# Performance work log

Measured on AMD Instinct MI355X. Metric: run time of the kernel, lower is better.

## Reference

```python
import jax, jax.numpy as jnp
import numpy as np


def _gcn(x, src, dst, W, b, M):
    # GCNConv: out = D^{-1/2} (A+I) D^{-1/2} X W + b, messages flow src->dst
    xw = x @ W  # [M, D]
    loops = jnp.arange(M)
    s = jnp.concatenate([src, loops])
    d = jnp.concatenate([dst, loops])
    deg = jax.ops.segment_sum(jnp.ones_like(s, x.dtype), d, num_segments=M)
    dinv = jnp.where(deg > 0, jax.lax.rsqrt(jnp.maximum(deg, 1.0)), 0.0)
    norm = dinv[s] * dinv[d]  # [Eg+M]
    return jax.ops.segment_sum(norm[:, None] * xw[s], d, num_segments=M) + b


def _graph_cross_attention(values, k, q, e_src, e_dst, N):
    # gather-dot, segment softmax over destination tokens, scatter-sum of values
    scale = jnp.sqrt(jnp.asarray(k.shape[1], k.dtype))
    dots = (q[e_dst] * k[e_src]).sum(-1) / scale  # [Ea]
    m = jax.ops.segment_max(dots, e_dst, num_segments=N)
    m = jnp.where(jnp.isfinite(m), m, 0.0)
    w = jnp.exp(dots - m[e_dst])
    den = jax.ops.segment_sum(w, e_dst, num_segments=N)
    w = w / jnp.where(den > 0, den, 1.0)[e_dst]
    return jax.ops.segment_sum(w[:, None] * values[e_src], e_dst, num_segments=N)


def reference(token_embeddings, tokens2edges, edge_index, e2t_src, e2t_dst,
              W_gnn, b_gnn, Wk, bk, Wq, bq, Wl, bl, gate_a, gate_b):
    N = token_embeddings.shape[1]
    M = tokens2edges.shape[1]

    def per_sample(t, t2e, ei, es, ed):
        edge_emb = t[t2e]                                  # [M, D] gather
        edge_emb = _gcn(edge_emb, ei[0], ei[1], W_gnn, b_gnn, M)
        k = edge_emb @ Wk + bk                             # [M, 64]
        q = t @ Wq + bq                                    # [N, 64]
        gatt = _graph_cross_attention(edge_emb, k, q, es, ed, N)  # [N, D]
        new = t + jnp.tanh(gate_a) * gatt
        new = new + jnp.tanh(gate_b) * (new @ Wl + bl)
        return new

    return jax.vmap(per_sample)(token_embeddings, tokens2edges, edge_index, e2t_src, e2t_dst)


def setup_inputs() -> dict:
    B, N, M, Eg, Ea, D, DK = 4, 4096, 16384, 65536, 65536, 512, 64
    key = jax.random.key(0)
    ks = jax.random.split(key, 16)
    s = 0.05  # weight scale to keep activations well-conditioned
    return {
        "token_embeddings": jax.random.normal(ks[0], (B, N, D), jnp.float32),
        "tokens2edges": jax.random.randint(ks[1], (B, M), 0, N),
        "edge_index": jax.random.randint(ks[2], (B, 2, Eg), 0, M),
        "e2t_src": jax.random.randint(ks[3], (B, Ea), 0, M),
        "e2t_dst": jax.random.randint(ks[4], (B, Ea), 0, N),
        "W_gnn": jax.random.normal(ks[5], (D, D), jnp.float32) * s,
        "b_gnn": jax.random.normal(ks[6], (D,), jnp.float32) * s,
        "Wk": jax.random.normal(ks[7], (D, DK), jnp.float32) * s,
        "bk": jax.random.normal(ks[8], (DK,), jnp.float32) * s,
        "Wq": jax.random.normal(ks[9], (D, DK), jnp.float32) * s,
        "bq": jax.random.normal(ks[10], (DK,), jnp.float32) * s,
        "Wl": jax.random.normal(ks[11], (D, D), jnp.float32) * s,
        "bl": jax.random.normal(ks[12], (D,), jnp.float32) * s,
        "gate_a": jax.random.normal(ks[13], (1,), jnp.float32),
        "gate_b": jax.random.normal(ks[14], (1,), jnp.float32),
    }
```

## Files before the change

### kernel.cpp

```cpp
#include <hip/hip_runtime.h>
#include <math.h>

#define BB 4
#define NT 4096
#define ME 16384
#define EG 65536
#define EA 65536
#define DD 512
#define DKK 64

using bf16x8 = __attribute__((ext_vector_type(8))) short;
using f32x4  = __attribute__((ext_vector_type(4))) float;

static __device__ __forceinline__ unsigned short f2bf(float f) {
    unsigned u = __float_as_uint(f);
    u += 0x7fffu + ((u >> 16) & 1u);
    return (unsigned short)(u >> 16);
}
static __device__ __forceinline__ float bf2f(unsigned short u) {
    return __uint_as_float((unsigned)u << 16);
}
static __device__ __forceinline__ void acc8(float* a, uint4 v, float s) {
    a[0] += s * __uint_as_float(v.x << 16);
    a[1] += s * __uint_as_float(v.x & 0xffff0000u);
    a[2] += s * __uint_as_float(v.y << 16);
    a[3] += s * __uint_as_float(v.y & 0xffff0000u);
    a[4] += s * __uint_as_float(v.z << 16);
    a[5] += s * __uint_as_float(v.z & 0xffff0000u);
    a[6] += s * __uint_as_float(v.w << 16);
    a[7] += s * __uint_as_float(v.w & 0xffff0000u);
}
static __device__ __forceinline__ uint4 pack8(const float* a) {
    uint4 o;
    o.x = (unsigned)f2bf(a[0]) | ((unsigned)f2bf(a[1]) << 16);
    o.y = (unsigned)f2bf(a[2]) | ((unsigned)f2bf(a[3]) << 16);
    o.z = (unsigned)f2bf(a[4]) | ((unsigned)f2bf(a[5]) << 16);
    o.w = (unsigned)f2bf(a[6]) | ((unsigned)f2bf(a[7]) << 16);
    return o;
}

__global__ void k_hist2(const int* __restrict__ ei_all, const int* __restrict__ ed_all,
                        int* __restrict__ cntG, int* __restrict__ cntA) {
    int i = blockIdx.x * 256 + threadIdx.x;
    if (i < BB * EG) {
        int b = i >> 16, e = i & (EG - 1);
        int dst = ei_all[(size_t)b * 2 * EG + EG + e];
        atomicAdd(&cntG[b * ME + dst], 1);
    } else {
        int j = i - BB * EG;
        atomicAdd(&cntA[(j >> 16) * NT + ed_all[j]], 1);
    }
}

__global__ __launch_bounds__(1024) void k_scan2(
    const int* __restrict__ cntG, int* __restrict__ offsG, int* __restrict__ curG,
    float* __restrict__ dinv,
    const int* __restrict__ cntA, int* __restrict__ offsA, int* __restrict__ curA) {
    __shared__ int sums[1024];
    int tid = threadIdx.x;
    int bid = blockIdx.x;
    const int* cnt;
    int *offs, *cur;
    float* dv = nullptr;
    int C, nk;
    if (bid < BB) {
        cnt = cntG + bid * ME; offs = offsG + bid * (ME + 1); cur = curG + bid * ME;
        dv = dinv + bid * ME; C = ME / 1024; nk = ME;
    } else {
        int b = bid - BB;
        cnt = cntA + b * NT; offs = offsA + b * (NT + 1); cur = curA + b * NT;
        C = NT / 1024; nk = NT;
    }
    int local[16];
    int tot = 0;
    for (int i = 0; i < C; ++i) { local[i] = cnt[tid * C + i]; tot += local[i]; }
    sums[tid] = tot;
    __syncthreads();
    for (int d = 1; d < 1024; d <<= 1) {
        int v = (tid >= d) ? sums[tid - d] : 0;
        __syncthreads();
        sums[tid] += v;
        __syncthreads();
    }
    int run = sums[tid] - tot;
    for (int i = 0; i < C; ++i) {
        int idx = tid * C + i;
        offs[idx] = run;
        cur[idx] = run;
        if (dv) dv[idx] = rsqrtf((float)local[i] + 1.0f);
        run += local[i];
    }
    if (tid == 1023) offs[nk] = run;
}

__global__ void k_fill2(const int* __restrict__ ei_all, const int* __restrict__ es_all,
                        const int* __restrict__ ed_all, const int* __restrict__ t2e_all,
                        const float* __restrict__ dinv,
                        int* __restrict__ curG, int2* __restrict__ csrG,
                        int* __restrict__ curA, int2* __restrict__ csrA) {
    int i = blockIdx.x * 256 + threadIdx.x;
    if (i < BB * EG) {
        int b = i >> 16, e = i & (EG - 1);
        const int* ei = ei_all + (size_t)b * 2 * EG;
        int s = ei[e], d = ei[EG + e];
        int p = atomicAdd(&curG[b * ME + d], 1);
        int2 v;
        v.x = t2e_all[(b << 14) + s];
        v.y = __float_as_int(dinv[b * ME + s]);
        csrG[(size_t)b * EG + p] = v;
    } else {
        int j = i - BB * EG;
        int b = j >> 16;
        int p = atomicAdd(&curA[b * NT + ed_all[j]], 1);
        int2 v;
        v.x = es_all[j];
        v.y = ed_all[j];
        csrA[(size_t)b * EA + p] = v;
    }
}

__global__ void k_cast(const float* __restrict__ x, unsigned short* __restrict__ xb) {
    long i = (long)blockIdx.x * blockDim.x + threadIdx.x;
    float4 v = *(const float4*)(x + (i << 2));
    ushort4 o;
    o.x = f2bf(v.x); o.y = f2bf(v.y); o.z = f2bf(v.z); o.w = f2bf(v.w);
    *(ushort4*)(xb + (i << 2)) = o;
}

__global__ void k_wt(const float* __restrict__ W, unsigned short* __restrict__ Wt) {
    int i = blockIdx.x * 256 + threadIdx.x;
    int n = i >> 9, k = i & 511;
    Wt[i] = f2bf(W[((long)k << 9) + n]);
}
__global__ void k_wtT(const float* __restrict__ Wgnn, const float* __restrict__ Wgk,
                      const float* __restrict__ Wq, unsigned short* __restrict__ BtT) {
    int i = blockIdx.x * 256 + threadIdx.x;
    int n = i >> 9, k = i & 511;
    float v;
    if (n < 512)      v = Wgnn[((long)k << 9) + n];
    else if (n < 576) v = Wgk[k * 64 + (n - 512)];
    else              v = Wq[k * 64 + (n - 576)];
    BtT[i] = f2bf(v);
}
__global__ void k_bias(const float* __restrict__ bgnn, const float* __restrict__ Wk,
                       const float* __restrict__ bk, const float* __restrict__ bq,
                       float* __restrict__ biasG, float* __restrict__ bias640) {
    int tid = threadIdx.x;
    if (tid < 512) { biasG[tid] = bgnn[tid]; bias640[tid] = 0.0f; return; }
    if (tid < 576) {
        int n = tid - 512;
        float s = bk[n];
        for (int k = 0; k < DD; ++k) s += bgnn[k] * Wk[k * 64 + n];
        biasG[tid] = s;
        bias640[tid] = 0.0f;
        return;
    }
    bias640[tid] = bq[tid - 576];
}

__global__ __launch_bounds__(256, 2) void gemm_token(
    const unsigned short* __restrict__ A, const unsigned short* __restrict__ BtT,
    const float* __restrict__ bias640, unsigned short* __restrict__ Xg,
    unsigned short* __restrict__ Xk, unsigned short* __restrict__ qmatb)
{
    __shared__ short As[64 * 32];
    __shared__ short Bs[320 * 32];
    int tid = threadIdx.x;
    int lane = tid & 63;
    int w = tid >> 6;
    long bm = (long)blockIdx.x * 64;
    int bcol = blockIdx.y * 320;
    const unsigned short* Bblk = BtT + (long)bcol * DD;

    f32x4 acc[4][5] = {};

    for (int k0 = 0; k0 < DD; k0 += 32) {
        {
            int s = tid;
            int r = s >> 2;
            int gc = ((s & 3) ^ ((s >> 3) & 3)) * 8;
            __builtin_amdgcn_global_load_lds(
                (const __attribute__((address_space(1))) unsigned int*)(A + (bm + r) * DD + k0 + gc),
                (__attribute__((address_space(3))) unsigned int*)(As + s * 8), 16, 0, 0);
        }
#pragma unroll
        for (int i = 0; i < 5; ++i) {
            int s = tid + i * 256;
            int r = s >> 2;
            int gc = ((s & 3) ^ ((s >> 3) & 3)) * 8;
            __builtin_amdgcn_global_load_lds(
                (const __attribute__((address_space(1))) unsigned int*)(Bblk + (long)r * DD + k0 + gc),
                (__attribute__((address_space(3))) unsigned int*)(Bs + s * 8), 16, 0, 0);
        }
        __syncthreads();

        int cq = lane >> 4;
        bf16x8 af[4];
#pragma unroll
        for (int rb = 0; rb < 4; ++rb) {
            int r = rb * 16 + (lane & 15);
            af[rb] = *(const bf16x8*)&As[(r * 4 + (cq ^ ((r >> 1) & 3))) * 8];
        }
#pragma unroll
        for (int cb = 0; cb < 5; ++cb) {
            int r = w * 80 + cb * 16 + (lane & 15);
            bf16x8 bf = *(const bf16x8*)&Bs[(r * 4 + (cq ^ ((r >> 1) & 3))) * 8];
#pragma unroll
            for (int rb = 0; rb < 4; ++rb)
                acc[rb][cb] = __builtin_amdgcn_mfma_f32_16x16x32_bf16(af[rb], bf, acc[rb][cb], 0, 0, 0);
        }
        __syncthreads();
    }

#pragma unroll
    for (int rb = 0; rb < 4; ++rb) {
        long row0 = bm + rb * 16 + ((lane >> 4) << 2);
#pragma unroll
        for (int cb = 0; cb < 5; ++cb) {
            int col = bcol + w * 80 + cb * 16 + (lane & 15);
            float bv = bias640[col];
            if (col < 512) {
#pragma unroll
                for (int r = 0; r < 4; ++r)
                    Xg[(row0 + r) * DD + col] = f2bf(acc[rb][cb][r] + bv);
            } else if (col < 576) {
#pragma unroll
                for (int r = 0; r < 4; ++r)
                    Xk[(row0 + r) * DKK + (col - 512)] = f2bf(acc[rb][cb][r] + bv);
            } else {
#pragma unroll
                for (int r = 0; r < 4; ++r)
                    qmatb[(row0 + r) * DKK + (col - 576)] = f2bf(acc[rb][cb][r] + bv);
            }
        }
    }
}

__global__ __launch_bounds__(256) void k_gcn_gather(
    const unsigned short* __restrict__ Xg, const unsigned short* __restrict__ Xk,
    const int* __restrict__ t2e_all, const float* __restrict__ dinv,
    const int* __restrict__ offsG, const int2* __restrict__ csrG,
    const float* __restrict__ biasG,
    unsigned short* __restrict__ eeb, unsigned short* __restrict__ kmatb)
{
    int mg = (blockIdx.x * 256 + threadIdx.x) >> 6;
    int lane = threadIdx.x & 63;
    int b = mg >> 14;
    int m = mg & (ME - 1);
    const int* offs = offsG + b * (ME + 1);
    const int2* csr = csrG + (size_t)b * EG;
    const unsigned short* gl = Xg + (((long)b * NT) << 9) + lane * 8;
    const unsigned short* kl = Xk + ((long)b * NT) * DKK + lane;

    float dm = dinv[mg];
    int self = t2e_all[mg];
    uint4 vself = *(const uint4*)(gl + ((long)self << 9));
    float kself = bf2f(kl[(long)self * DKK]);

    float a[8] = {0, 0, 0, 0, 0, 0, 0, 0};
    float ak = 0.0f;
    int p = offs[m], end = offs[m + 1];
    for (; p + 4 <= end; p += 4) {
        int2 e0 = csr[p], e1 = csr[p + 1], e2 = csr[p + 2], e3 = csr[p + 3];
        uint4 r0 = *(const uint4*)(gl + ((long)e0.x << 9));
        uint4 r1 = *(const uint4*)(gl + ((long)e1.x << 9));
        uint4 r2 = *(const uint4*)(gl + ((long)e2.x << 9));
        uint4 r3 = *(const uint4*)(gl + ((long)e3.x << 9));
        float k0 = bf2f(kl[(long)e0.x * DKK]);
        float k1 = bf2f(kl[(long)e1.x * DKK]);
        float k2 = bf2f(kl[(long)e2.x * DKK]);
        float k3 = bf2f(kl[(long)e3.x * DKK]);
        float w0 = __int_as_float(e0.y), w1 = __int_as_float(e1.y);
        float w2 = __int_as_float(e2.y), w3 = __int_as_float(e3.y);
        acc8(a, r0, w0); ak += w0 * k0;
        acc8(a, r1, w1); ak += w1 * k1;
        acc8(a, r2, w2); ak += w2 * k2;
        acc8(a, r3, w3); ak += w3 * k3;
    }
    if (p < end) {
        int e1m = end - 1;
        int i1 = min(p + 1, e1m), i2 = min(p + 2, e1m), i3 = min(p + 3, e1m);
        int2 e0 = csr[p], e1 = csr[i1], e2 = csr[i2], e3 = csr[i3];
        uint4 r0 = *(const uint4*)(gl + ((long)e0.x << 9));
        uint4 r1 = *(const uint4*)(gl + ((long)e1.x << 9));
        uint4 r2 = *(const uint4*)(gl + ((long)e2.x << 9));
        uint4 r3 = *(const uint4*)(gl + ((long)e3.x << 9));
        float k0 = bf2f(kl[(long)e0.x * DKK]);
        float k1 = bf2f(kl[(long)e1.x * DKK]);
        float k2 = bf2f(kl[(long)e2.x * DKK]);
        float k3 = bf2f(kl[(long)e3.x * DKK]);
        float w0 = __int_as_float(e0.y);
        float w1 = (p + 1 < end) ? __int_as_float(e1.y) : 0.0f;
        float w2 = (p + 2 < end) ? __int_as_float(e2.y) : 0.0f;
        float w3 = (p + 3 < end) ? __int_as_float(e3.y) : 0.0f;
        acc8(a, r0, w0); ak += w0 * k0;
        acc8(a, r1, w1); ak += w1 * k1;
        acc8(a, r2, w2); ak += w2 * k2;
        acc8(a, r3, w3); ak += w3 * k3;
    }
    acc8(a, vself, dm);
    ak += dm * kself;

    const float* bg = biasG + lane * 8;
    float4 b0 = *(const float4*)bg;
    float4 b1 = *(const float4*)(bg + 4);
    a[0] = dm * a[0] + b0.x; a[1] = dm * a[1] + b0.y;
    a[2] = dm * a[2] + b0.z; a[3] = dm * a[3] + b0.w;
    a[4] = dm * a[4] + b1.x; a[5] = dm * a[5] + b1.y;
    a[6] = dm * a[6] + b1.z; a[7] = dm * a[7] + b1.w;
    *(uint4*)(eeb + ((long)mg << 9) + lane * 8) = pack8(a);
    kmatb[(long)mg * DKK + lane] = f2bf(dm * ak + biasG[512 + lane]);
}

__global__ void k_dots(const unsigned short* __restrict__ kmatb,
                       const unsigned short* __restrict__ qmatb,
                       const int2* __restrict__ csrA, int2* __restrict__ swbuf) {
    int p = blockIdx.x * 256 + threadIdx.x;
    int b = p >> 16;
    int2 sd = csrA[p];
    const uint4* kr = (const uint4*)(kmatb + ((long)(b * ME + sd.x) << 6));
    const uint4* qr = (const uint4*)(qmatb + ((long)(b * NT + sd.y) << 6));
    float dot = 0.0f;
#pragma unroll
    for (int j = 0; j < 8; ++j) {
        uint4 kv = kr[j];
        uint4 qv = qr[j];
        dot += __uint_as_float(kv.x << 16) * __uint_as_float(qv.x << 16)
             + __uint_as_float(kv.x & 0xffff0000u) * __uint_as_float(qv.x & 0xffff0000u)
             + __uint_as_float(kv.y << 16) * __uint_as_float(qv.y << 16)
             + __uint_as_float(kv.y & 0xffff0000u) * __uint_as_float(qv.y & 0xffff0000u)
             + __uint_as_float(kv.z << 16) * __uint_as_float(qv.z << 16)
             + __uint_as_float(kv.z & 0xffff0000u) * __uint_as_float(qv.z & 0xffff0000u)
             + __uint_as_float(kv.w << 16) * __uint_as_float(qv.w << 16)
             + __uint_as_float(kv.w & 0xffff0000u) * __uint_as_float(qv.w & 0xffff0000u);
    }
    int2 o;
    o.x = sd.x;
    o.y = __float_as_int(expf(dot * 0.125f));
    swbuf[p] = o;
}

__global__ __launch_bounds__(256) void k_att_gather(
    const unsigned short* __restrict__ eeb, const int2* __restrict__ swbuf,
    const int* __restrict__ offsA,
    const float* __restrict__ t_all, const float* __restrict__ ga,
    float* __restrict__ out, unsigned short* __restrict__ nb)
{
    int ng = (blockIdx.x * 256 + threadIdx.x) >> 6;
    int lane = threadIdx.x & 63;
    int b = ng >> 12;
    int n = ng & (NT - 1);
    const int* offs = offsA + b * (NT + 1);
    const int2* swb = swbuf + (size_t)b * EA;
    const unsigned short* el = eeb + (((size_t)b * ME) << 9) + lane * 8;

    float a[8] = {0, 0, 0, 0, 0, 0, 0, 0};
    float den = 0.0f;
    int p = offs[n], end = offs[n + 1];
    for (; p + 8 <= end; p += 8) {
        int2 e0 = swb[p],     e1 = swb[p + 1], e2 = swb[p + 2], e3 = swb[p + 3];
        int2 e4 = swb[p + 4], e5 = swb[p + 5], e6 = swb[p + 6], e7 = swb[p + 7];
        uint4 r0 = *(const uint4*)(el + ((long)e0.x << 9));
        uint4 r1 = *(const uint4*)(el + ((long)e1.x << 9));
        uint4 r2 = *(const uint4*)(el + ((long)e2.x << 9));
        uint4 r3 = *(const uint4*)(el + ((long)e3.x << 9));
        uint4 r4 = *(const uint4*)(el + ((long)e4.x << 9));
        uint4 r5 = *(const uint4*)(el + ((long)e5.x << 9));
        uint4 r6 = *(const uint4*)(el + ((long)e6.x << 9));
        uint4 r7 = *(const uint4*)(el + ((long)e7.x << 9));
        float w0 = __int_as_float(e0.y), w1 = __int_as_float(e1.y);
        float w2 = __int_as_float(e2.y), w3 = __int_as_float(e3.y);
        float w4 = __int_as_float(e4.y), w5 = __int_as_float(e5.y);
        float w6 = __int_as_float(e6.y), w7 = __int_as_float(e7.y);
        den += (w0 + w1 + w2 + w3) + (w4 + w5 + w6 + w7);
        acc8(a, r0, w0);
        acc8(a, r1, w1);
        acc8(a, r2, w2);
        acc8(a, r3, w3);
        acc8(a, r4, w4);
        acc8(a, r5, w5);
        acc8(a, r6, w6);
        acc8(a, r7, w7);
    }
    if (p < end) {
        int e1m = end - 1;
        int2 e0 = swb[p];
        int2 e1 = swb[min(p + 1, e1m)];
        int2 e2 = swb[min(p + 2, e1m)];
        int2 e3 = swb[min(p + 3, e1m)];
        int2 e4 = swb[min(p + 4, e1m)];
        int2 e5 = swb[min(p + 5, e1m)];
        int2 e6 = swb[min(p + 6, e1m)];
        int2 e7 = swb[min(p + 7, e1m)];
        uint4 r0 = *(const uint4*)(el + ((long)e0.x << 9));
        uint4 r1 = *(const uint4*)(el + ((long)e1.x << 9));
        uint4 r2 = *(const uint4*)(el + ((long)e2.x << 9));
        uint4 r3 = *(const uint4*)(el + ((long)e3.x << 9));
        uint4 r4 = *(const uint4*)(el + ((long)e4.x << 9));
        uint4 r5 = *(const uint4*)(el + ((long)e5.x << 9));
        uint4 r6 = *(const uint4*)(el + ((long)e6.x << 9));
        uint4 r7 = *(const uint4*)(el + ((long)e7.x << 9));
        float w0 = __int_as_float(e0.y);
        float w1 = (p + 1 < end) ? __int_as_float(e1.y) : 0.0f;
        float w2 = (p + 2 < end) ? __int_as_float(e2.y) : 0.0f;
        float w3 = (p + 3 < end) ? __int_as_float(e3.y) : 0.0f;
        float w4 = (p + 4 < end) ? __int_as_float(e4.y) : 0.0f;
        float w5 = (p + 5 < end) ? __int_as_float(e5.y) : 0.0f;
        float w6 = (p + 6 < end) ? __int_as_float(e6.y) : 0.0f;
        float w7 = (p + 7 < end) ? __int_as_float(e7.y) : 0.0f;
        den += (w0 + w1 + w2 + w3) + (w4 + w5 + w6 + w7);
        acc8(a, r0, w0);
        acc8(a, r1, w1);
        acc8(a, r2, w2);
        acc8(a, r3, w3);
        acc8(a, r4, w4);
        acc8(a, r5, w5);
        acc8(a, r6, w6);
        acc8(a, r7, w7);
    }
    float g = tanhf(ga[0]);
    float inv = den > 0.0f ? g / den : 0.0f;
    const float* tr = t_all + ((long)ng << 9) + lane * 8;
    float4 t0 = *(const float4*)tr;
    float4 t1 = *(const float4*)(tr + 4);
    float o[8];
    o[0] = t0.x + inv * a[0]; o[1] = t0.y + inv * a[1];
    o[2] = t0.z + inv * a[2]; o[3] = t0.w + inv * a[3];
    o[4] = t1.x + inv * a[4]; o[5] = t1.y + inv * a[5];
    o[6] = t1.z + inv * a[6]; o[7] = t1.w + inv * a[7];
    float* op = out + ((long)ng << 9) + lane * 8;
    *(float4*)op = make_float4(o[0], o[1], o[2], o[3]);
    *(float4*)(op + 4) = make_float4(o[4], o[5], o[6], o[7]);
    *(uint4*)(nb + ((long)ng << 9) + lane * 8) = pack8(o);
}

__global__ __launch_bounds__(256, 2) void gemm_final(
    const unsigned short* __restrict__ A, const unsigned short* __restrict__ Bt,
    const float* __restrict__ bias, float* __restrict__ Cf, const float* __restrict__ gs)
{
    constexpr int CB = 8;
    constexpr int BROWS = 2 * CB * 16;
    __shared__ short As[128 * 32];
    __shared__ short Bs[BROWS * 32];
    int tid = threadIdx.x;
    int lane = tid & 63;
    int w = tid >> 6;
    int wm = w >> 1, wn = w & 1;
    long bm = (long)blockIdx.x * 128;
    int bcol = blockIdx.y * BROWS;
    const unsigned short* Bblk = Bt + (long)bcol * DD;

    f32x4 acc[4][CB] = {};

    for (int k0 = 0; k0 < DD; k0 += 32) {
#pragma unroll
        for (int i = 0; i < 2; ++i) {
            int s = tid + i * 256;
            int r = s >> 2;
            int gc = ((s & 3) ^ ((s >> 3) & 3)) * 8;
            __builtin_amdgcn_global_load_lds(
                (const __attribute__((address_space(1))) unsigned int*)(A + (bm + r) * DD + k0 + gc),
                (__attribute__((address_space(3))) unsigned int*)(As + s * 8), 16, 0, 0);
        }
#pragma unroll
        for (int i = 0; i < CB / 2; ++i) {
            int s = tid + i * 256;
            int r = s >> 2;
            int gc = ((s & 3) ^ ((s >> 3) & 3)) * 8;
            __builtin_amdgcn_global_load_lds(
                (const __attribute__((address_space(1))) unsigned int*)(Bblk + (long)r * DD + k0 + gc),
                (__attribute__((address_space(3))) unsigned int*)(Bs + s * 8), 16, 0, 0);
        }
        __syncthreads();

        int cq = lane >> 4;
        bf16x8 af[4];
#pragma unroll
        for (int rb = 0; rb < 4; ++rb) {
            int r = wm * 64 + rb * 16 + (lane & 15);
            af[rb] = *(const bf16x8*)&As[(r * 4 + (cq ^ ((r >> 1) & 3))) * 8];
        }
#pragma unroll
        for (int cb = 0; cb < CB; ++cb) {
            int r = wn * (CB * 16) + cb * 16 + (lane & 15);
            bf16x8 bf = *(const bf16x8*)&Bs[(r * 4 + (cq ^ ((r >> 1) & 3))) * 8];
#pragma unroll
            for (int rb = 0; rb < 4; ++rb)
                acc[rb][cb] = __builtin_amdgcn_mfma_f32_16x16x32_bf16(af[rb], bf, acc[rb][cb], 0, 0, 0);
        }
        __syncthreads();
    }

    float g = tanhf(gs[0]);
#pragma unroll
    for (int rb = 0; rb < 4; ++rb) {
        long row0 = bm + wm * 64 + rb * 16 + ((lane >> 4) << 2);
#pragma unroll
        for (int cb = 0; cb < CB; ++cb) {
            int col = bcol + wn * (CB * 16) + cb * 16 + (lane & 15);
            float bv = bias[col];
#pragma unroll
            for (int r = 0; r < 4; ++r)
                Cf[(row0 + r) * DD + col] += g * (acc[rb][cb][r] + bv);
        }
    }
}

__global__ void gemm_tiled(const float* __restrict__ A, const float* __restrict__ Bw,
                           float* __restrict__ C, int K, int Nc) {
    __shared__ float As[16][64];
    __shared__ float Bs[16][64];
    int tid = threadIdx.x;
    int tx = tid & 15, ty = tid >> 4;
    int bm = blockIdx.x * 64, bn = blockIdx.y * 64;
    float acc[4][4] = {};
    int arow = bm + (tid >> 2);
    long aoff = (long)arow * K;
    int kk0 = (tid & 3) * 4;
    int arowl = tid >> 2;
    for (int k0 = 0; k0 < K; k0 += 16) {
        float4 av = *(const float4*)(A + aoff + k0 + kk0);
        As[kk0 + 0][arowl] = av.x;
        As[kk0 + 1][arowl] = av.y;
        As[kk0 + 2][arowl] = av.z;
        As[kk0 + 3][arowl] = av.w;
        float4 bv = *(const float4*)(Bw + (long)(k0 + (tid >> 4)) * Nc + bn + (tid & 15) * 4);
        *(float4*)&Bs[tid >> 4][(tid & 15) * 4] = bv;
        __syncthreads();
#pragma unroll
        for (int k = 0; k < 16; ++k) {
            float4 a = *(const float4*)&As[k][ty * 4];
            float4 b = *(const float4*)&Bs[k][tx * 4];
            acc[0][0] += a.x * b.x; acc[0][1] += a.x * b.y; acc[0][2] += a.x * b.z; acc[0][3] += a.x * b.w;
            acc[1][0] += a.y * b.x; acc[1][1] += a.y * b.y; acc[1][2] += a.y * b.z; acc[1][3] += a.y * b.w;
            acc[2][0] += a.z * b.x; acc[2][1] += a.z * b.y; acc[2][2] += a.z * b.z; acc[2][3] += a.z * b.w;
            acc[3][0] += a.w * b.x; acc[3][1] += a.w * b.y; acc[3][2] += a.w * b.z; acc[3][3] += a.w * b.w;
        }
        __syncthreads();
    }
#pragma unroll
    for (int i = 0; i < 4; ++i)
        *(float4*)(C + (long)(bm + ty * 4 + i) * Nc + bn + tx * 4) =
            make_float4(acc[i][0], acc[i][1], acc[i][2], acc[i][3]);
}

extern "C" void kernel_launch(void* const* d_in, const int* in_sizes, int n_in,
                              void* d_out, int out_size, void* d_ws, size_t ws_size,
                              hipStream_t stream) {
    const float* t_all   = (const float*)d_in[0];
    const int*   t2e_all = (const int*)d_in[1];
    const int*   ei_all  = (const int*)d_in[2];
    const int*   es_all  = (const int*)d_in[3];
    const int*   ed_all  = (const int*)d_in[4];
    const float* Wgnn    = (const float*)d_in[5];
    const float* bgnn    = (const float*)d_in[6];
    const float* Wk      = (const float*)d_in[7];
    const float* bk      = (const float*)d_in[8];
    const float* Wq      = (const float*)d_in[9];
    const float* bq      = (const float*)d_in[10];
    const float* Wl      = (const float*)d_in[11];
    const float* bl      = (const float*)d_in[12];
    const float* ga      = (const float*)d_in[13];
    const float* gb      = (const float*)d_in[14];
    float* out = (float*)d_out;

    char* wsb = (char*)d_ws;
    size_t off = 0;
    unsigned short* eeb   = (unsigned short*)(wsb + off); off += (size_t)BB * ME * DD * 2;
    unsigned short* tb    = (unsigned short*)(wsb + off); off += (size_t)BB * NT * DD * 2;
    unsigned short* Xg    = (unsigned short*)(wsb + off); off += (size_t)BB * NT * DD * 2;
    unsigned short* nb    = (unsigned short*)(wsb + off); off += (size_t)BB * NT * DD * 2;
    unsigned short* Xk    = (unsigned short*)(wsb + off); off += (size_t)BB * NT * DKK * 2;
    unsigned short* qmatb = (unsigned short*)(wsb + off); off += (size_t)BB * NT * DKK * 2;
    unsigned short* kmatb = (unsigned short*)(wsb + off); off += (size_t)BB * ME * DKK * 2;
    unsigned short* BtT   = (unsigned short*)(wsb + off); off += (size_t)640 * DD * 2;
    unsigned short* Wlt   = (unsigned short*)(wsb + off); off += (size_t)DD * DD * 2;
    float* Wgk     = (float*)(wsb + off); off += (size_t)DD * DKK * 4;
    float* biasG   = (float*)(wsb + off); off += 576 * 4;
    float* bias640 = (float*)(wsb + off); off += 640 * 4;
    float* dinv  = (float*)(wsb + off); off += (size_t)BB * ME * 4;
    int2* swbuf  = (int2*)(wsb + off); off += (size_t)BB * EA * 8;
    int* cntG  = (int*)(wsb + off); off += (size_t)BB * ME * 4;
    int* cntA  = (int*)(wsb + off); off += (size_t)BB * NT * 4;
    int* offsG = (int*)(wsb + off); off += (size_t)BB * (ME + 1) * 4;
    int* curG  = (int*)(wsb + off); off += (size_t)BB * ME * 4;
    int2* csrG = (int2*)(wsb + off); off += (size_t)BB * EG * 8;
    int* offsA = (int*)(wsb + off); off += (size_t)BB * (NT + 1) * 4;
    int* curA  = (int*)(wsb + off); off += (size_t)BB * NT * 4;
    int2* csrA = (int2*)(wsb + off); off += (size_t)BB * EA * 8;

    gemm_tiled<<<dim3(DD / 64, 1), 256, 0, stream>>>(Wgnn, Wk, Wgk, DD, DKK);
    k_wt<<<(DD * DD) / 256, 256, 0, stream>>>(Wl, Wlt);
    k_wtT<<<(640 * DD) / 256, 256, 0, stream>>>(Wgnn, Wgk, Wq, BtT);
    k_bias<<<1, 640, 0, stream>>>(bgnn, Wk, bk, bq, biasG, bias640);

    hipMemsetAsync(cntG, 0, (size_t)BB * (ME + NT) * 4, stream);
    k_hist2<<<(BB * (EG + EA)) / 256, 256, 0, stream>>>(ei_all, ed_all, cntG, cntA);
    k_scan2<<<2 * BB, 1024, 0, stream>>>(cntG, offsG, curG, dinv, cntA, offsA, curA);
    k_fill2<<<(BB * (EG + EA)) / 256, 256, 0, stream>>>(
        ei_all, es_all, ed_all, t2e_all, dinv, curG, csrG, curA, csrA);

    k_cast<<<(int)(((long)BB * NT * DD / 4) / 256), 256, 0, stream>>>(t_all, tb);
    gemm_token<<<dim3((BB * NT) / 64, 2), 256, 0, stream>>>(tb, BtT, bias640, Xg, Xk, qmatb);

    k_gcn_gather<<<(BB * ME * 64) / 256, 256, 0, stream>>>(
        Xg, Xk, t2e_all, dinv, offsG, csrG, biasG, eeb, kmatb);

    k_dots<<<(BB * EA) / 256, 256, 0, stream>>>(kmatb, qmatb, csrA, swbuf);
    k_att_gather<<<(BB * NT * 64) / 256, 256, 0, stream>>>(
        eeb, swbuf, offsA, t_all, ga, out, nb);

    gemm_final<<<dim3((BB * NT) / 128, 2), 256, 0, stream>>>(nb, Wlt, bl, out, gb);
}
```

Before: 390.6 us.

## Fuse weight preprocessing kernels and remap block indices for batch-local scheduling

Merges the small Wgnn·Wk GEMM, both weight transposes and the Wl transpose into a single preprocessing kernel. The Wgnn·Wk product is now computed inline per element with a serial 512-length dot product. The bias kernel is split across 67 blocks, with a shared-memory tree reduction for the k-bias. The GCN gather and dot kernels remap blockIdx so that consecutive blocks are interleaved across batches and halves, which is meant to change cache locality and XCD distribution. The aims are fewer launches and better L2 reuse, at the cost of redundant inline dot-product work for 64×512 elements.

```diff
diff --git a/kernel.cpp b/kernel.cpp
--- a/kernel.cpp
+++ b/kernel.cpp
@@ -127,35 +127,52 @@
     *(ushort4*)(xb + (i << 2)) = o;
 }
 
-__global__ void k_wt(const float* __restrict__ W, unsigned short* __restrict__ Wt) {
+__global__ void k_wtT(const float* __restrict__ Wgnn, const float* __restrict__ Wk,
+                      const float* __restrict__ Wq, const float* __restrict__ Wl,
+                      unsigned short* __restrict__ BtT, unsigned short* __restrict__ Wlt) {
     int i = blockIdx.x * 256 + threadIdx.x;
-    int n = i >> 9, k = i & 511;
-    Wt[i] = f2bf(W[((long)k << 9) + n]);
-}
-__global__ void k_wtT(const float* __restrict__ Wgnn, const float* __restrict__ Wgk,
-                      const float* __restrict__ Wq, unsigned short* __restrict__ BtT) {
-    int i = blockIdx.x * 256 + threadIdx.x;
-    int n = i >> 9, k = i & 511;
-    float v;
-    if (n < 512)      v = Wgnn[((long)k << 9) + n];
-    else if (n < 576) v = Wgk[k * 64 + (n - 512)];
-    else              v = Wq[k * 64 + (n - 576)];
-    BtT[i] = f2bf(v);
-}
-__global__ void k_bias(const float* __restrict__ bgnn, const float* __restrict__ Wk,
-                       const float* __restrict__ bk, const float* __restrict__ bq,
-                       float* __restrict__ biasG, float* __restrict__ bias640) {
-    int tid = threadIdx.x;
-    if (tid < 512) { biasG[tid] = bgnn[tid]; bias640[tid] = 0.0f; return; }
-    if (tid < 576) {
-        int n = tid - 512;
-        float s = bk[n];
-        for (int k = 0; k < DD; ++k) s += bgnn[k] * Wk[k * 64 + n];
-        biasG[tid] = s;
-        bias640[tid] = 0.0f;
+    if (i < 640 * 512) {
+        int n = i >> 9, k = i & 511;
+        float v;
+        if (n < 512)      v = Wgnn[((long)k << 9) + n];
+        else if (n < 576) {
+            int c = n - 512;
+            const float* wr = Wgnn + ((long)k << 9);
+            float s = 0.0f;
+            for (int j = 0; j < DD; ++j) s += wr[j] * Wk[j * 64 + c];
+            v = s;
+        } else            v = Wq[k * 64 + (n - 576)];
+        BtT[i] = f2bf(v);
+    } else {
+        int j = i - 640 * 512;
+        int n = j >> 9, k = j & 511;
+        Wlt[j] = f2bf(Wl[((long)k << 9) + n]);
+    }
+}
+
+__global__ __launch_bounds__(256) void k_bias(
+    const float* __restrict__ bgnn, const float* __restrict__ Wk,
+    const float* __restrict__ bk, const float* __restrict__ bq,
+    float* __restrict__ biasG, float* __restrict__ bias640) {
+    int bx = blockIdx.x, tid = threadIdx.x;
+    if (bx < 3) {
+        int i = bx * 256 + tid;
+        if (i < 512) { biasG[i] = bgnn[i]; bias640[i] = 0.0f; }
+        else if (i < 576) { bias640[i] = 0.0f; }
+        else if (i < 640) { bias640[i] = bq[i - 576]; }
         return;
     }
-    bias640[tid] = bq[tid - 576];
+    int n = bx - 3;
+    __shared__ float red[256];
+    float s = 0.0f;
+    for (int k = tid; k < DD; k += 256) s += bgnn[k] * Wk[k * 64 + n];
+    red[tid] = s;
+    __syncthreads();
+    for (int d = 128; d > 0; d >>= 1) {
+        if (tid < d) red[tid] += red[tid + d];
+        __syncthreads();
+    }
+    if (tid == 0) biasG[512 + n] = red[0] + bk[n];
 }
 
 __global__ __launch_bounds__(256, 2) void gemm_token(
@@ -243,10 +260,14 @@
     const float* __restrict__ biasG,
     unsigned short* __restrict__ eeb, unsigned short* __restrict__ kmatb)
 {
-    int mg = (blockIdx.x * 256 + threadIdx.x) >> 6;
+    int w = threadIdx.x >> 6;
     int lane = threadIdx.x & 63;
-    int b = mg >> 14;
-    int m = mg & (ME - 1);
+    int bx = blockIdx.x;
+    int b = (bx & 7) >> 1;
+    int half = bx & 1;
+    int idx = bx >> 3;
+    int m = (half * 2048 + idx) * 4 + w;
+    int mg = (b << 14) + m;
     const int* offs = offsG + b * (ME + 1);
     const int2* csr = csrG + (size_t)b * EG;
     const unsigned short* gl = Xg + (((long)b * NT) << 9) + lane * 8;
@@ -315,8 +336,11 @@
 __global__ void k_dots(const unsigned short* __restrict__ kmatb,
                        const unsigned short* __restrict__ qmatb,
                        const int2* __restrict__ csrA, int2* __restrict__ swbuf) {
-    int p = blockIdx.x * 256 + threadIdx.x;
-    int b = p >> 16;
+    int bx = blockIdx.x;
+    int b = (bx & 7) >> 1;
+    int half = bx & 1;
+    int idx = bx >> 3;
+    int p = (b << 16) + (half * 128 + idx) * 256 + threadIdx.x;
     int2 sd = csrA[p];
     const uint4* kr = (const uint4*)(kmatb + ((long)(b * ME + sd.x) << 6));
     const uint4* qr = (const uint4*)(qmatb + ((long)(b * NT + sd.y) << 6));
@@ -506,44 +530,6 @@
     }
 }
 
-__global__ void gemm_tiled(const float* __restrict__ A, const float* __restrict__ Bw,
-                           float* __restrict__ C, int K, int Nc) {
-    __shared__ float As[16][64];
-    __shared__ float Bs[16][64];
-    int tid = threadIdx.x;
-    int tx = tid & 15, ty = tid >> 4;
-    int bm = blockIdx.x * 64, bn = blockIdx.y * 64;
-    float acc[4][4] = {};
-    int arow = bm + (tid >> 2);
-    long aoff = (long)arow * K;
-    int kk0 = (tid & 3) * 4;
-    int arowl = tid >> 2;
-    for (int k0 = 0; k0 < K; k0 += 16) {
-        float4 av = *(const float4*)(A + aoff + k0 + kk0);
-        As[kk0 + 0][arowl] = av.x;
-        As[kk0 + 1][arowl] = av.y;
-        As[kk0 + 2][arowl] = av.z;
-        As[kk0 + 3][arowl] = av.w;
-        float4 bv = *(const float4*)(Bw + (long)(k0 + (tid >> 4)) * Nc + bn + (tid & 15) * 4);
-        *(float4*)&Bs[tid >> 4][(tid & 15) * 4] = bv;
-        __syncthreads();
-#pragma unroll
-        for (int k = 0; k < 16; ++k) {
-            float4 a = *(const float4*)&As[k][ty * 4];
-            float4 b = *(const float4*)&Bs[k][tx * 4];
-            acc[0][0] += a.x * b.x; acc[0][1] += a.x * b.y; acc[0][2] += a.x * b.z; acc[0][3] += a.x * b.w;
-            acc[1][0] += a.y * b.x; acc[1][1] += a.y * b.y; acc[1][2] += a.y * b.z; acc[1][3] += a.y * b.w;
-            acc[2][0] += a.z * b.x; acc[2][1] += a.z * b.y; acc[2][2] += a.z * b.z; acc[2][3] += a.z * b.w;
-            acc[3][0] += a.w * b.x; acc[3][1] += a.w * b.y; acc[3][2] += a.w * b.z; acc[3][3] += a.w * b.w;
-        }
-        __syncthreads();
-    }
-#pragma unroll
-    for (int i = 0; i < 4; ++i)
-        *(float4*)(C + (long)(bm + ty * 4 + i) * Nc + bn + tx * 4) =
-            make_float4(acc[i][0], acc[i][1], acc[i][2], acc[i][3]);
-}
-
 extern "C" void kernel_launch(void* const* d_in, const int* in_sizes, int n_in,
                               void* d_out, int out_size, void* d_ws, size_t ws_size,
                               hipStream_t stream) {
@@ -575,7 +561,6 @@
     unsigned short* kmatb = (unsigned short*)(wsb + off); off += (size_t)BB * ME * DKK * 2;
     unsigned short* BtT   = (unsigned short*)(wsb + off); off += (size_t)640 * DD * 2;
     unsigned short* Wlt   = (unsigned short*)(wsb + off); off += (size_t)DD * DD * 2;
-    float* Wgk     = (float*)(wsb + off); off += (size_t)DD * DKK * 4;
     float* biasG   = (float*)(wsb + off); off += 576 * 4;
     float* bias640 = (float*)(wsb + off); off += 640 * 4;
     float* dinv  = (float*)(wsb + off); off += (size_t)BB * ME * 4;
@@ -589,10 +574,8 @@
     int* curA  = (int*)(wsb + off); off += (size_t)BB * NT * 4;
     int2* csrA = (int2*)(wsb + off); off += (size_t)BB * EA * 8;
 
-    gemm_tiled<<<dim3(DD / 64, 1), 256, 0, stream>>>(Wgnn, Wk, Wgk, DD, DKK);
-    k_wt<<<(DD * DD) / 256, 256, 0, stream>>>(Wl, Wlt);
-    k_wtT<<<(640 * DD) / 256, 256, 0, stream>>>(Wgnn, Wgk, Wq, BtT);
-    k_bias<<<1, 640, 0, stream>>>(bgnn, Wk, bk, bq, biasG, bias640);
+    k_wtT<<<(1152 * DD) / 256, 256, 0, stream>>>(Wgnn, Wk, Wq, Wl, BtT, Wlt);
+    k_bias<<<67, 256, 0, stream>>>(bgnn, Wk, bk, bq, biasG, bias640);
 
     hipMemsetAsync(cntG, 0, (size_t)BB * (ME + NT) * 4, stream);
     k_hist2<<<(BB * (EG + EA)) / 256, 256, 0, stream>>>(ei_all, ed_all, cntG, cntA);
```

Result: faster. 361.0 us (-7.6%).
